# Kernel tuning notes

Hardware: AMD Instinct MI355X
Metric: run time of the kernel (lower is better)

Reference implementation:

```python
import jax, jax.numpy as jnp
import numpy as np

BLOCK = 32  # GGUF Q8_0 block size


def setup_inputs() -> dict:
    key = jax.random.key(0)
    k1, k2, k3, k4 = jax.random.split(key, 4)
    O, I = 11008, 4096
    x = jax.random.normal(k1, (32, I), dtype=jnp.float32)
    qweight = jax.random.randint(k2, (O, I), 0, 255, dtype=jnp.int32)
    scales = jax.random.uniform(k3, (O, I // BLOCK), dtype=jnp.float32) * 0.01
    bias = jax.random.normal(k4, (O,), dtype=jnp.float32)
    return {"x": x, "qweight": qweight, "scales": scales, "bias": bias}


def dequantize(qweight, scales):
    # Q8_0-style: signed int8 quants, one fp scale per block of 32 along in-dim.
    O, I = qweight.shape
    q = (qweight.astype(scales.dtype) - 127.0).reshape(O, I // BLOCK, BLOCK)
    w = q * scales[:, :, None]  # [O, nb, BLOCK]
    return w.reshape(O, I)


def reference(x, qweight, scales, bias):
    # On-the-fly dequant fused with F.linear: y = x @ W^T + b
    w = dequantize(qweight, scales)           # [O, I]
    return jnp.einsum('bi,oi->bo', x, w) + bias
```

## Files before the change

kernel.cpp:

```cpp
#include <hip/hip_runtime.h>
#include <hip/hip_bf16.h>


#define O_DIM  11008
#define I_DIM  4096
#define NB     128
#define B_DIM  32
#define NSPLIT 16
#define KT     (I_DIM / NSPLIT)
#define PART_STRIDE (O_DIM * B_DIM)

typedef __attribute__((ext_vector_type(8))) short bf16x8;
typedef __attribute__((ext_vector_type(8))) unsigned short u16x8;
typedef __attribute__((ext_vector_type(4))) float f32x4;
typedef __attribute__((ext_vector_type(4))) int   i32x4;

static __device__ __forceinline__ unsigned short f2bf(float f) {
    return __builtin_bit_cast(unsigned short, __float2bfloat16(f));
}

static __device__ __forceinline__ unsigned int pkf16(float a, float b) {
    const unsigned short ua = __builtin_bit_cast(unsigned short, (_Float16)a);
    const unsigned short ub = __builtin_bit_cast(unsigned short, (_Float16)b);
    return (unsigned int)ua | ((unsigned int)ub << 16);
}

static __device__ __forceinline__ bf16x8 dequant8(const i32x4 qa, const i32x4 qb,
                                                  const float s) {
    const float c = -127.0f * s;
    bf16x8 v;
    v[0] = (short)f2bf(fmaf((float)qa[0], s, c));
    v[1] = (short)f2bf(fmaf((float)qa[1], s, c));
    v[2] = (short)f2bf(fmaf((float)qa[2], s, c));
    v[3] = (short)f2bf(fmaf((float)qa[3], s, c));
    v[4] = (short)f2bf(fmaf((float)qb[0], s, c));
    v[5] = (short)f2bf(fmaf((float)qb[1], s, c));
    v[6] = (short)f2bf(fmaf((float)qb[2], s, c));
    v[7] = (short)f2bf(fmaf((float)qb[3], s, c));
    return v;
}

__global__ __launch_bounds__(256) void gemm_kernel(const float* __restrict__ x,
                                                   const int*   __restrict__ qw,
                                                   const float* __restrict__ scales,
                                                   unsigned short* __restrict__ part) {
    __shared__ unsigned short x_s[B_DIM * KT];

    const int t    = threadIdx.x;
    const int wav  = t >> 6;
    const int lan  = t & 63;
    const int lrow = lan & 15;
    const int lq   = lan >> 4;

    const int split  = blockIdx.x;
    const int k_base = split * KT;
    const int o_row  = blockIdx.y * 64 + wav * 16 + lrow;

    const int* __restrict__ wq = qw + o_row * I_DIM + k_base + lq * 8;

    float sc[8];
    {
        const float4* sp = reinterpret_cast<const float4*>(&scales[o_row * NB + split * 8]);
        const float4 s0 = sp[0], s1 = sp[1];
        sc[0] = s0.x; sc[1] = s0.y; sc[2] = s0.z; sc[3] = s0.w;
        sc[4] = s1.x; sc[5] = s1.y; sc[6] = s1.z; sc[7] = s1.w;
    }

    i32x4 wa0, wb0, wc0, wd0, wa1, wb1, wc1, wd1, wa2, wb2, wc2, wd2;

#define LOADW(A, B, C, D, c) {                           \
        const int* wp = wq + (c) * 64;                   \
        A = *reinterpret_cast<const i32x4*>(wp);         \
        B = *reinterpret_cast<const i32x4*>(wp + 4);     \
        C = *reinterpret_cast<const i32x4*>(wp + 32);    \
        D = *reinterpret_cast<const i32x4*>(wp + 36); }

    LOADW(wa0, wb0, wc0, wd0, 0)
    LOADW(wa1, wb1, wc1, wd1, 1)

    {
        const int m  = t >> 3;
        const int k0 = (t & 7) * 32;
        const float4* xv = reinterpret_cast<const float4*>(x + m * I_DIM + k_base + k0);
#pragma unroll
        for (int j = 0; j < 4; ++j) {
            const float4 va = xv[2 * j];
            const float4 vb = xv[2 * j + 1];
            bf16x8 v;
            v[0] = (short)f2bf(va.x); v[1] = (short)f2bf(va.y);
            v[2] = (short)f2bf(va.z); v[3] = (short)f2bf(va.w);
            v[4] = (short)f2bf(vb.x); v[5] = (short)f2bf(vb.y);
            v[6] = (short)f2bf(vb.z); v[7] = (short)f2bf(vb.w);
            const int addr = ((m * KT + k0 + j * 8) * 2) ^ ((m & 7) << 4);
            *reinterpret_cast<bf16x8*>(reinterpret_cast<char*>(x_s) + addr) = v;
        }
    }

    __syncthreads();

    f32x4 acc0 = {0.f, 0.f, 0.f, 0.f};
    f32x4 acc1 = {0.f, 0.f, 0.f, 0.f};
    const int swz = (lrow & 7) << 4;

#define CONSUME(A, B, C, D, c) {                                                              \
        const int kb = (c) * 64 + lq * 8;                                                     \
        const bf16x8 a0 = *reinterpret_cast<const bf16x8*>(                                   \
            reinterpret_cast<const char*>(x_s) + ((( lrow       * KT + kb) * 2) ^ swz));      \
        const bf16x8 a1 = *reinterpret_cast<const bf16x8*>(                                   \
            reinterpret_cast<const char*>(x_s) + ((((lrow + 16) * KT + kb) * 2) ^ swz));      \
        const bf16x8 bA = dequant8(A, B, sc[2 * (c)]);                                        \
        acc0 = __builtin_amdgcn_mfma_f32_16x16x32_bf16(a0, bA, acc0, 0, 0, 0);                \
        acc1 = __builtin_amdgcn_mfma_f32_16x16x32_bf16(a1, bA, acc1, 0, 0, 0);                \
        const bf16x8 a2 = *reinterpret_cast<const bf16x8*>(                                   \
            reinterpret_cast<const char*>(x_s) + ((( lrow       * KT + kb + 32) * 2) ^ swz)); \
        const bf16x8 a3 = *reinterpret_cast<const bf16x8*>(                                   \
            reinterpret_cast<const char*>(x_s) + ((((lrow + 16) * KT + kb + 32) * 2) ^ swz)); \
        const bf16x8 bB = dequant8(C, D, sc[2 * (c) + 1]);                                    \
        acc0 = __builtin_amdgcn_mfma_f32_16x16x32_bf16(a2, bB, acc0, 0, 0, 0);                \
        acc1 = __builtin_amdgcn_mfma_f32_16x16x32_bf16(a3, bB, acc1, 0, 0, 0); }

    LOADW(wa2, wb2, wc2, wd2, 2)
    CONSUME(wa0, wb0, wc0, wd0, 0)
    LOADW(wa0, wb0, wc0, wd0, 3)
    CONSUME(wa1, wb1, wc1, wd1, 1)
    CONSUME(wa2, wb2, wc2, wd2, 2)
    CONSUME(wa0, wb0, wc0, wd0, 3)

#undef LOADW
#undef CONSUME

    unsigned short* pp = part + split * PART_STRIDE + o_row * B_DIM;
    const uint2 v0 = make_uint2(pkf16(acc0[0], acc0[1]), pkf16(acc0[2], acc0[3]));
    const uint2 v1 = make_uint2(pkf16(acc1[0], acc1[1]), pkf16(acc1[2], acc1[3]));
    *reinterpret_cast<uint2*>(&pp[lq * 4])      = v0;
    *reinterpret_cast<uint2*>(&pp[16 + lq * 4]) = v1;
}

__global__ __launch_bounds__(256) void reduce_kernel(const unsigned short* __restrict__ part,
                                                     const float* __restrict__ bias,
                                                     float* __restrict__ out) {
    const int o = blockIdx.x * 256 + threadIdx.x;
    float v[B_DIM];
#pragma unroll
    for (int m = 0; m < B_DIM; ++m) v[m] = 0.f;

#pragma unroll
    for (int s = 0; s < NSPLIT; ++s) {
        const unsigned short* ps = part + s * PART_STRIDE + o * B_DIM;
#pragma unroll
        for (int g = 0; g < 4; ++g) {
            const u16x8 p = *reinterpret_cast<const u16x8*>(ps + g * 8);
#pragma unroll
            for (int j = 0; j < 8; ++j)
                v[g * 8 + j] += (float)__builtin_bit_cast(_Float16, (unsigned short)p[j]);
        }
    }

    const float b = bias[o];
#pragma unroll
    for (int m = 0; m < B_DIM; ++m)
        out[m * O_DIM + o] = v[m] + b;
}

extern "C" void kernel_launch(void* const* d_in, const int* in_sizes, int n_in,
                              void* d_out, int out_size, void* d_ws, size_t ws_size,
                              hipStream_t stream) {
    const float* x      = (const float*)d_in[0];
    const int*   qw     = (const int*)d_in[1];
    const float* scales = (const float*)d_in[2];
    const float* bias   = (const float*)d_in[3];
    float*       out    = (float*)d_out;
    unsigned short* part = (unsigned short*)d_ws;

    hipLaunchKernelGGL(gemm_kernel, dim3(NSPLIT, O_DIM / 64), dim3(256), 0, stream,
                       x, qw, scales, part);

    hipLaunchKernelGGL(reduce_kernel, dim3(O_DIM / 256), dim3(256), 0, stream,
                       part, bias, out);
}
```

Baseline: 48.07 us.

## Stage quantized weights into LDS via direct global-to-LDS loads and double K-splits

```diff
diff --git a/kernel.cpp b/kernel.cpp
--- a/kernel.cpp
+++ b/kernel.cpp
@@ -6,7 +6,7 @@
 #define I_DIM  4096
 #define NB     128
 #define B_DIM  32
-#define NSPLIT 16
+#define NSPLIT 32
 #define KT     (I_DIM / NSPLIT)
 #define PART_STRIDE (O_DIM * B_DIM)
 
@@ -23,6 +23,13 @@
     const unsigned short ua = __builtin_bit_cast(unsigned short, (_Float16)a);
     const unsigned short ub = __builtin_bit_cast(unsigned short, (_Float16)b);
     return (unsigned int)ua | ((unsigned int)ub << 16);
+}
+
+static __device__ __forceinline__ void gl_lds16(const void* g, void* l) {
+    __builtin_amdgcn_global_load_lds(
+        (const __attribute__((address_space(1))) void*)g,
+        (__attribute__((address_space(3))) void*)l,
+        16, 0, 0);
 }
 
 static __device__ __forceinline__ bf16x8 dequant8(const i32x4 qa, const i32x4 qb,
@@ -44,6 +51,7 @@
                                                    const int*   __restrict__ qw,
                                                    const float* __restrict__ scales,
                                                    unsigned short* __restrict__ part) {
+    __shared__ int            w_s[64 * KT];
     __shared__ unsigned short x_s[B_DIM * KT];
 
     const int t    = threadIdx.x;
@@ -54,36 +62,31 @@
 
     const int split  = blockIdx.x;
     const int k_base = split * KT;
-    const int o_row  = blockIdx.y * 64 + wav * 16 + lrow;
+    const int o_wave = blockIdx.y * 64 + wav * 16;
+    const int o_row  = o_wave + lrow;
 
-    const int* __restrict__ wq = qw + o_row * I_DIM + k_base + lq * 8;
-
-    float sc[8];
     {
-        const float4* sp = reinterpret_cast<const float4*>(&scales[o_row * NB + split * 8]);
-        const float4 s0 = sp[0], s1 = sp[1];
-        sc[0] = s0.x; sc[1] = s0.y; sc[2] = s0.z; sc[3] = s0.w;
-        sc[4] = s1.x; sc[5] = s1.y; sc[6] = s1.z; sc[7] = s1.w;
+        const int  half = lan >> 5;
+        const int  li   = lan & 31;
+        char*       ldsb = (char*)w_s + wav * 8192;
+        const char* gb   = (const char*)(qw + (size_t)o_wave * I_DIM + k_base);
+#pragma unroll
+        for (int j = 0; j < 8; ++j) {
+            const int rl  = 2 * j + half;
+            const int off = (li * 16) ^ ((rl & 7) << 4);
+            gl_lds16(gb + (size_t)rl * (I_DIM * 4) + off, ldsb + j * 1024);
+        }
     }
 
-    i32x4 wa0, wb0, wc0, wd0, wa1, wb1, wc1, wd1, wa2, wb2, wc2, wd2;
-
-#define LOADW(A, B, C, D, c) {                           \
-        const int* wp = wq + (c) * 64;                   \
-        A = *reinterpret_cast<const i32x4*>(wp);         \
-        B = *reinterpret_cast<const i32x4*>(wp + 4);     \
-        C = *reinterpret_cast<const i32x4*>(wp + 32);    \
-        D = *reinterpret_cast<const i32x4*>(wp + 36); }
-
-    LOADW(wa0, wb0, wc0, wd0, 0)
-    LOADW(wa1, wb1, wc1, wd1, 1)
+    const float4 scv = *reinterpret_cast<const float4*>(&scales[o_row * NB + split * 4]);
+    const float sc[4] = {scv.x, scv.y, scv.z, scv.w};
 
     {
         const int m  = t >> 3;
-        const int k0 = (t & 7) * 32;
+        const int k0 = (t & 7) * 16;
         const float4* xv = reinterpret_cast<const float4*>(x + m * I_DIM + k_base + k0);
 #pragma unroll
-        for (int j = 0; j < 4; ++j) {
+        for (int j = 0; j < 2; ++j) {
             const float4 va = xv[2 * j];
             const float4 vb = xv[2 * j + 1];
             bf16x8 v;
@@ -101,35 +104,25 @@
     f32x4 acc0 = {0.f, 0.f, 0.f, 0.f};
     f32x4 acc1 = {0.f, 0.f, 0.f, 0.f};
     const int swz = (lrow & 7) << 4;
+    const char* wbase = (const char*)w_s + wav * 8192 + lrow * 512;
+    const char* xbase = (const char*)x_s;
 
-#define CONSUME(A, B, C, D, c) {                                                              \
-        const int kb = (c) * 64 + lq * 8;                                                     \
-        const bf16x8 a0 = *reinterpret_cast<const bf16x8*>(                                   \
-            reinterpret_cast<const char*>(x_s) + ((( lrow       * KT + kb) * 2) ^ swz));      \
-        const bf16x8 a1 = *reinterpret_cast<const bf16x8*>(                                   \
-            reinterpret_cast<const char*>(x_s) + ((((lrow + 16) * KT + kb) * 2) ^ swz));      \
-        const bf16x8 bA = dequant8(A, B, sc[2 * (c)]);                                        \
-        acc0 = __builtin_amdgcn_mfma_f32_16x16x32_bf16(a0, bA, acc0, 0, 0, 0);                \
-        acc1 = __builtin_amdgcn_mfma_f32_16x16x32_bf16(a1, bA, acc1, 0, 0, 0);                \
-        const bf16x8 a2 = *reinterpret_cast<const bf16x8*>(                                   \
-            reinterpret_cast<const char*>(x_s) + ((( lrow       * KT + kb + 32) * 2) ^ swz)); \
-        const bf16x8 a3 = *reinterpret_cast<const bf16x8*>(                                   \
-            reinterpret_cast<const char*>(x_s) + ((((lrow + 16) * KT + kb + 32) * 2) ^ swz)); \
-        const bf16x8 bB = dequant8(C, D, sc[2 * (c) + 1]);                                    \
-        acc0 = __builtin_amdgcn_mfma_f32_16x16x32_bf16(a2, bB, acc0, 0, 0, 0);                \
-        acc1 = __builtin_amdgcn_mfma_f32_16x16x32_bf16(a3, bB, acc1, 0, 0, 0); }
+#pragma unroll
+    for (int ks = 0; ks < 4; ++ks) {
+        const int off = ks * 128 + lq * 32;
+        const i32x4 qlo = *reinterpret_cast<const i32x4*>(wbase + ((off)      ^ swz));
+        const i32x4 qhi = *reinterpret_cast<const i32x4*>(wbase + ((off + 16) ^ swz));
+        const int kb2 = (ks * 32 + lq * 8) * 2;
+        const bf16x8 a0 = *reinterpret_cast<const bf16x8*>(
+            xbase + (( lrow       * 256 + kb2) ^ swz));
+        const bf16x8 a1 = *reinterpret_cast<const bf16x8*>(
+            xbase + (((lrow + 16) * 256 + kb2) ^ swz));
+        const bf16x8 bf = dequant8(qlo, qhi, sc[ks]);
+        acc0 = __builtin_amdgcn_mfma_f32_16x16x32_bf16(a0, bf, acc0, 0, 0, 0);
+        acc1 = __builtin_amdgcn_mfma_f32_16x16x32_bf16(a1, bf, acc1, 0, 0, 0);
+    }
 
-    LOADW(wa2, wb2, wc2, wd2, 2)
-    CONSUME(wa0, wb0, wc0, wd0, 0)
-    LOADW(wa0, wb0, wc0, wd0, 3)
-    CONSUME(wa1, wb1, wc1, wd1, 1)
-    CONSUME(wa2, wb2, wc2, wd2, 2)
-    CONSUME(wa0, wb0, wc0, wd0, 3)
-
-#undef LOADW
-#undef CONSUME
-
-    unsigned short* pp = part + split * PART_STRIDE + o_row * B_DIM;
+    unsigned short* pp = part + (size_t)split * PART_STRIDE + o_row * B_DIM;
     const uint2 v0 = make_uint2(pkf16(acc0[0], acc0[1]), pkf16(acc0[2], acc0[3]));
     const uint2 v1 = make_uint2(pkf16(acc1[0], acc1[1]), pkf16(acc1[2], acc1[3]));
     *reinterpret_cast<uint2*>(&pp[lq * 4])      = v0;
@@ -144,9 +137,8 @@
 #pragma unroll
     for (int m = 0; m < B_DIM; ++m) v[m] = 0.f;
 
-#pragma unroll
     for (int s = 0; s < NSPLIT; ++s) {
-        const unsigned short* ps = part + s * PART_STRIDE + o * B_DIM;
+        const unsigned short* ps = part + (size_t)s * PART_STRIDE + o * B_DIM;
 #pragma unroll
         for (int g = 0; g < 4; ++g) {
             const u16x8 p = *reinterpret_cast<const u16x8*>(ps + g * 8);
```

Measured after the change: 49.93 us. 1.04x slower.

## Replace split-K partial buffer and reduce kernel with atomic accumulation

Applied to the files above, without the earlier changes.

```diff
diff --git a/kernel.cpp b/kernel.cpp
--- a/kernel.cpp
+++ b/kernel.cpp
@@ -8,21 +8,13 @@
 #define B_DIM  32
 #define NSPLIT 16
 #define KT     (I_DIM / NSPLIT)
-#define PART_STRIDE (O_DIM * B_DIM)
 
 typedef __attribute__((ext_vector_type(8))) short bf16x8;
-typedef __attribute__((ext_vector_type(8))) unsigned short u16x8;
 typedef __attribute__((ext_vector_type(4))) float f32x4;
 typedef __attribute__((ext_vector_type(4))) int   i32x4;
 
 static __device__ __forceinline__ unsigned short f2bf(float f) {
     return __builtin_bit_cast(unsigned short, __float2bfloat16(f));
-}
-
-static __device__ __forceinline__ unsigned int pkf16(float a, float b) {
-    const unsigned short ua = __builtin_bit_cast(unsigned short, (_Float16)a);
-    const unsigned short ub = __builtin_bit_cast(unsigned short, (_Float16)b);
-    return (unsigned int)ua | ((unsigned int)ub << 16);
 }
 
 static __device__ __forceinline__ bf16x8 dequant8(const i32x4 qa, const i32x4 qb,
@@ -40,10 +32,19 @@
     return v;
 }
 
+__global__ __launch_bounds__(256) void bias_fill_kernel(const float* __restrict__ bias,
+                                                        float* __restrict__ out) {
+    const int idx = blockIdx.x * 256 + threadIdx.x;
+    const int m   = idx / (O_DIM / 4);
+    const int o4  = (idx - m * (O_DIM / 4)) * 4;
+    const f32x4 b = *reinterpret_cast<const f32x4*>(&bias[o4]);
+    *reinterpret_cast<f32x4*>(&out[(size_t)m * O_DIM + o4]) = b;
+}
+
 __global__ __launch_bounds__(256) void gemm_kernel(const float* __restrict__ x,
                                                    const int*   __restrict__ qw,
                                                    const float* __restrict__ scales,
-                                                   unsigned short* __restrict__ part) {
+                                                   float*       __restrict__ out) {
     __shared__ unsigned short x_s[B_DIM * KT];
 
     const int t    = threadIdx.x;
@@ -56,7 +57,7 @@
     const int k_base = split * KT;
     const int o_row  = blockIdx.y * 64 + wav * 16 + lrow;
 
-    const int* __restrict__ wq = qw + o_row * I_DIM + k_base + lq * 8;
+    const int* __restrict__ wq = qw + (size_t)o_row * I_DIM + k_base + lq * 8;
 
     float sc[8];
     {
@@ -129,37 +130,12 @@
 #undef LOADW
 #undef CONSUME
 
-    unsigned short* pp = part + split * PART_STRIDE + o_row * B_DIM;
-    const uint2 v0 = make_uint2(pkf16(acc0[0], acc0[1]), pkf16(acc0[2], acc0[3]));
-    const uint2 v1 = make_uint2(pkf16(acc1[0], acc1[1]), pkf16(acc1[2], acc1[3]));
-    *reinterpret_cast<uint2*>(&pp[lq * 4])      = v0;
-    *reinterpret_cast<uint2*>(&pp[16 + lq * 4]) = v1;
-}
-
-__global__ __launch_bounds__(256) void reduce_kernel(const unsigned short* __restrict__ part,
-                                                     const float* __restrict__ bias,
-                                                     float* __restrict__ out) {
-    const int o = blockIdx.x * 256 + threadIdx.x;
-    float v[B_DIM];
 #pragma unroll
-    for (int m = 0; m < B_DIM; ++m) v[m] = 0.f;
-
-#pragma unroll
-    for (int s = 0; s < NSPLIT; ++s) {
-        const unsigned short* ps = part + s * PART_STRIDE + o * B_DIM;
-#pragma unroll
-        for (int g = 0; g < 4; ++g) {
-            const u16x8 p = *reinterpret_cast<const u16x8*>(ps + g * 8);
-#pragma unroll
-            for (int j = 0; j < 8; ++j)
-                v[g * 8 + j] += (float)__builtin_bit_cast(_Float16, (unsigned short)p[j]);
-        }
+    for (int r = 0; r < 4; ++r) {
+        const int m = lq * 4 + r;
+        atomicAdd(&out[(size_t)m * O_DIM + o_row],        acc0[r]);
+        atomicAdd(&out[(size_t)(m + 16) * O_DIM + o_row], acc1[r]);
     }
-
-    const float b = bias[o];
-#pragma unroll
-    for (int m = 0; m < B_DIM; ++m)
-        out[m * O_DIM + o] = v[m] + b;
 }
 
 extern "C" void kernel_launch(void* const* d_in, const int* in_sizes, int n_in,
@@ -170,11 +146,10 @@
     const float* scales = (const float*)d_in[2];
     const float* bias   = (const float*)d_in[3];
     float*       out    = (float*)d_out;
-    unsigned short* part = (unsigned short*)d_ws;
+
+    hipLaunchKernelGGL(bias_fill_kernel, dim3((B_DIM * O_DIM / 4) / 256), dim3(256),
+                       0, stream, bias, out);
 
     hipLaunchKernelGGL(gemm_kernel, dim3(NSPLIT, O_DIM / 64), dim3(256), 0, stream,
-                       x, qw, scales, part);
-
-    hipLaunchKernelGGL(reduce_kernel, dim3(O_DIM / 256), dim3(256), 0, stream,
-                       part, bias, out);
+                       x, qw, scales, out);
 }
```

Measured after the change: 51.31 us. +6.7%, slower.
